# Kernel tuning notes

Hardware: AMD Instinct MI355X
Metric: run time of the kernel (lower is better)

Reference implementation:

```python
import jax, jax.numpy as jnp
import numpy as np

C = 256
NUM_HEADS = 8
EPS = 1e-5


def setup_inputs() -> dict:
    key = jax.random.key(0)
    ks = jax.random.split(key, 8)
    x = jax.random.normal(ks[0], (2, C, 64, 64), dtype=jnp.float32)
    # LayerNorm params (torch default: weight=1, bias=0)
    norm_w = jnp.ones((C,), jnp.float32)
    norm_b = jnp.zeros((C,), jnp.float32)
    # qkv Linear: weight (3C, C), bias (3C,)
    qkv_w = jax.random.normal(ks[1], (3 * C, C), dtype=jnp.float32) * (1.0 / np.sqrt(C))
    qkv_b = jax.random.normal(ks[2], (3 * C,), dtype=jnp.float32) * 0.01
    # proj Linear: weight (C, C), bias (C,)
    proj_w = jax.random.normal(ks[3], (C, C), dtype=jnp.float32) * (1.0 / np.sqrt(C))
    proj_b = jax.random.normal(ks[4], (C,), dtype=jnp.float32) * 0.01
    # gamma initialized to zeros in torch, but use small nonzero so output depends on attention
    gamma = jnp.full((1,), 0.1, jnp.float32)
    return {"x": x, "norm_w": norm_w, "norm_b": norm_b, "qkv_w": qkv_w,
            "qkv_b": qkv_b, "proj_w": proj_w, "proj_b": proj_b, "gamma": gamma}


def reference(x, norm_w, norm_b, qkv_w, qkv_b, proj_w, proj_b, gamma):
    B, Cc, H, W = x.shape
    N = H * W
    nh = NUM_HEADS
    hd = Cc // nh
    scale = hd ** (-0.5)

    # (B, N, C)
    x_flat = x.reshape(B, Cc, N).transpose(0, 2, 1)

    # LayerNorm over last dim
    mu = jnp.mean(x_flat, axis=-1, keepdims=True)
    var = jnp.mean(jnp.square(x_flat - mu), axis=-1, keepdims=True)
    x_norm = (x_flat - mu) * jax.lax.rsqrt(var + EPS) * norm_w + norm_b

    # QKV projection: (B, N, 3C) -> (3, B, nh, N, hd)
    qkv = x_norm @ qkv_w.T + qkv_b
    qkv = qkv.reshape(B, N, 3, nh, hd).transpose(2, 0, 3, 1, 4)
    q, k, v = qkv[0], qkv[1], qkv[2]

    # attention scores (B, nh, N, N); note torch code scales AFTER q@k.T
    attn = jnp.einsum('bhnd,bhmd->bhnm', q, k) * scale
    attn = jax.nn.softmax(attn, axis=-1)

    # (B, nh, N, hd) -> (B, N, C)
    x_attn = jnp.einsum('bhnm,bhmd->bhnd', attn, v)
    x_attn = x_attn.transpose(0, 2, 1, 3).reshape(B, N, Cc)
    x_attn = x_attn @ proj_w.T + proj_b

    # back to (B, C, H, W) and scaled residual
    x_attn = x_attn.transpose(0, 2, 1).reshape(B, Cc, H, W)
    return gamma * x_attn + x
```

## Files before the change

kernel.cpp:

```cpp
#include <hip/hip_runtime.h>

#define CCH   256
#define NSEQ  4096
#define NH    8
#define HD    32

typedef short s8x __attribute__((ext_vector_type(8)));
typedef float f4x __attribute__((ext_vector_type(4)));

__device__ __forceinline__ f4x mfma16(s8x a, s8x b, f4x c) {
  return __builtin_amdgcn_mfma_f32_16x16x32_bf16(a, b, c, 0, 0, 0);
}

__device__ __forceinline__ unsigned short f2bf(float f) {
  union { float f; unsigned int u; } v; v.f = f;
  unsigned int u = v.u + 0x7fffu + ((v.u >> 16) & 1u);
  return (unsigned short)(u >> 16);
}

__device__ __forceinline__ unsigned int pk_bf_rnd(float lo, float hi) {
  return (unsigned int)f2bf(lo) | ((unsigned int)f2bf(hi) << 16);
}

__device__ __forceinline__ unsigned int pk_bf_trunc(float lo, float hi) {
  union { float f; unsigned int u; } a, b; a.f = lo; b.f = hi;
  return __builtin_amdgcn_perm(b.u, a.u, 0x07060302);
}

#if defined(__has_builtin)
#if __has_builtin(__builtin_amdgcn_exp2f)
#define FEXP2(x) __builtin_amdgcn_exp2f(x)
#endif
#endif
#ifndef FEXP2
__device__ __forceinline__ float __fexp2_asm(float x) {
  float r; asm("v_exp_f32 %0, %1" : "=v"(r) : "v"(x)); return r;
}
#define FEXP2(x) __fexp2_asm(x)
#endif

#define C2SCALE (0.17677669529663689f * 1.4426950408889634f)

__global__ __launch_bounds__(256) void ln_cvt_kernel(const float* __restrict__ x,
                                                     const float* __restrict__ nw,
                                                     const float* __restrict__ nb,
                                                     unsigned short* __restrict__ xn,
                                                     const float* __restrict__ qw,
                                                     const float* __restrict__ pw,
                                                     unsigned short* __restrict__ qwb,
                                                     unsigned short* __restrict__ pwb) {
  if (blockIdx.x >= 256) {
    const int t = (blockIdx.x - 256) * 256 + threadIdx.x;
    const float4* src;
    unsigned short* dst;
    int idx;
    if (t < 49152) { src = reinterpret_cast<const float4*>(qw); dst = qwb; idx = t; }
    else           { src = reinterpret_cast<const float4*>(pw); dst = pwb; idx = t - 49152; }
    const float4 vv = src[idx];
    union { unsigned short u[4]; uint2 v; } pk;
    pk.u[0] = f2bf(vv.x); pk.u[1] = f2bf(vv.y); pk.u[2] = f2bf(vv.z); pk.u[3] = f2bf(vv.w);
    *reinterpret_cast<uint2*>(dst + 4 * idx) = pk.v;
    return;
  }

  __shared__ float Ls[256 * 32];
  __shared__ float Sred[2][32][8];
  __shared__ float Mrs[32][2];
  const int t  = threadIdx.x;
  const int n  = t & 31;
  const int cg = t >> 5;
  const int p0 = blockIdx.x * 32;
  const int b  = p0 >> 12;
  const int n0 = p0 & 4095;
  const float* xb = x + (size_t)b * CCH * NSEQ + n0;

  #pragma unroll
  for (int i = 0; i < 32; ++i) {
    const int c = i * 8 + cg;
    Ls[c * 32 + (n ^ (c & 31))] = xb[(size_t)c * NSEQ + n];
  }
  __syncthreads();

  float s = 0.f, sq = 0.f;
  #pragma unroll
  for (int j = 0; j < 32; ++j) {
    const int c = cg * 32 + j;
    const float v = Ls[c * 32 + (n ^ j)];
    s += v; sq += v * v;
  }
  Sred[0][n][cg] = s; Sred[1][n][cg] = sq;
  __syncthreads();
  float ts = 0.f, tq = 0.f;
  #pragma unroll
  for (int g = 0; g < 8; ++g) { ts += Sred[0][n][g]; tq += Sred[1][n][g]; }
  const float mean = ts * (1.f / 256.f);
  const float rstd = rsqrtf(tq * (1.f / 256.f) - mean * mean + 1e-5f);
  if (cg == 0) { Mrs[n][0] = mean; Mrs[n][1] = rstd; }
  __syncthreads();

  const int n2  = t >> 3;
  const int c8b = t & 7;
  const float mean2 = Mrs[n2][0];
  const float rstd2 = Mrs[n2][1];
  unsigned short* orow = xn + ((size_t)b * NSEQ + n0 + n2) * CCH;
  #pragma unroll
  for (int j8 = 0; j8 < 4; ++j8) {
    const int cb = (j8 * 8 + c8b) * 8;
    unsigned int w_[4];
    #pragma unroll
    for (int hw = 0; hw < 4; ++hw) {
      const int c = cb + hw * 2;
      const float v0 = Ls[c * 32 + (n2 ^ (c & 31))];
      const float v1 = Ls[(c + 1) * 32 + (n2 ^ ((c + 1) & 31))];
      const float y0 = (v0 - mean2) * rstd2 * nw[c] + nb[c];
      const float y1 = (v1 - mean2) * rstd2 * nw[c + 1] + nb[c + 1];
      w_[hw] = pk_bf_rnd(y0, y1);
    }
    uint4 pkv; pkv.x = w_[0]; pkv.y = w_[1]; pkv.z = w_[2]; pkv.w = w_[3];
    *reinterpret_cast<uint4*>(orow + cb) = pkv;
  }
}

#define GEMM_CORE(A_PTR, B_PTR, ACC)                                            \
  {                                                                             \
    for (int kb = 0; kb < 4; ++kb) {                                            \
      if (kb) __syncthreads();                                                  \
      _Pragma("unroll")                                                         \
      for (int j = 0; j < 4; ++j) {                                             \
        const int c = j * 256 + tid;                                            \
        const int ar = c >> 3, acr = c & 7;                                     \
        *reinterpret_cast<s8x*>(&As[ar * 64 + ((acr ^ (ar & 7)) << 3)]) =       \
          *reinterpret_cast<const s8x*>(A_PTR + (size_t)(mt * 128 + ar) * CCH + kb * 64 + acr * 8); \
      }                                                                         \
      _Pragma("unroll")                                                         \
      for (int j = 0; j < 2; ++j) {                                             \
        const int c = j * 256 + tid;                                            \
        const int br = c >> 3, bcr = c & 7;                                     \
        *reinterpret_cast<s8x*>(&Bs[br * 64 + ((bcr ^ (br & 7)) << 3)]) =       \
          *reinterpret_cast<const s8x*>(B_PTR + (size_t)(nt * 64 + br) * CCH + kb * 64 + bcr * 8); \
      }                                                                         \
      __syncthreads();                                                          \
      _Pragma("unroll")                                                         \
      for (int kin = 0; kin < 2; ++kin) {                                       \
        const int chx = ((kin * 4 + quad) ^ (l16 & 7)) << 3;                    \
        const s8x a0 = *reinterpret_cast<const s8x*>(&As[(wv * 32 + l16) * 64 + chx]);      \
        const s8x a1 = *reinterpret_cast<const s8x*>(&As[(wv * 32 + 16 + l16) * 64 + chx]); \
        _Pragma("unroll")                                                       \
        for (int ni = 0; ni < 4; ++ni) {                                        \
          const s8x bf = *reinterpret_cast<const s8x*>(&Bs[(ni * 16 + l16) * 64 + chx]);    \
          ACC[0][ni] = mfma16(a0, bf, ACC[0][ni]);                              \
          ACC[1][ni] = mfma16(a1, bf, ACC[1][ni]);                              \
        }                                                                       \
      }                                                                         \
    }                                                                           \
  }

__global__ __launch_bounds__(256, 3) void qkv_gemm(const unsigned short* __restrict__ xn,
                                                   const unsigned short* __restrict__ w,
                                                   const float* __restrict__ bias,
                                                   unsigned short* __restrict__ q,
                                                   unsigned short* __restrict__ k,
                                                   unsigned short* __restrict__ vt) {
  __shared__ unsigned short As[128 * 64];
  __shared__ unsigned short Bs[64 * 64];
  __shared__ unsigned short Ts[128 * 72];
  const int tid = threadIdx.x;
  const int wv  = tid >> 6;
  const int lane = tid & 63;
  const int quad = lane >> 4, l16 = lane & 15;
  const int mt = blockIdx.x;
  const int nt = blockIdx.y;

  f4x acc[2][4];
  #pragma unroll
  for (int mi = 0; mi < 2; ++mi)
    #pragma unroll
    for (int ni = 0; ni < 4; ++ni)
      acc[mi][ni] = (f4x){0.f, 0.f, 0.f, 0.f};

  GEMM_CORE(xn, w, acc)

  const int sel = nt >> 2;
  if (sel == 2) {
    #pragma unroll
    for (int ni = 0; ni < 4; ++ni) {
      const int o = nt * 64 + ni * 16 + l16;
      const float bs = bias[o];
      const int ol = o & 255;
      const int head = ol >> 5, d = ol & 31;
      #pragma unroll
      for (int mi = 0; mi < 2; ++mi) {
        const int g0 = mt * 128 + wv * 32 + mi * 16 + quad * 4;
        const int bb = g0 >> 12, n0 = g0 & 4095;
        unsigned short* vp = vt + ((size_t)(bb * NH + head) * HD + d) * NSEQ + n0;
        uint2 pk;
        pk.x = pk_bf_rnd(acc[mi][ni][0] + bs, acc[mi][ni][1] + bs);
        pk.y = pk_bf_rnd(acc[mi][ni][2] + bs, acc[mi][ni][3] + bs);
        *reinterpret_cast<uint2*>(vp) = pk;
      }
    }
  } else {
    const float sc = (sel == 0) ? C2SCALE : 1.f;
    unsigned short* base = (sel == 0) ? q : k;
    #pragma unroll
    for (int ni = 0; ni < 4; ++ni) {
      const int o = nt * 64 + ni * 16 + l16;
      const float bs = bias[o];
      const int oc = ni * 16 + l16;
      #pragma unroll
      for (int mi = 0; mi < 2; ++mi) {
        const int nl = wv * 32 + mi * 16 + quad * 4;
        #pragma unroll
        for (int r = 0; r < 4; ++r)
          Ts[(nl + r) * 72 + oc] = f2bf((acc[mi][ni][r] + bs) * sc);
      }
    }
    const int n2 = tid >> 1;
    const int hh = tid & 1;
    const int head = 2 * (nt & 3) + hh;
    const int g = mt * 128 + n2;
    const int bb = g >> 12, n0g = g & 4095;
    unsigned short* dst = base + ((size_t)(bb * NH + head) * NSEQ + n0g) * HD;
    #pragma unroll
    for (int j = 0; j < 4; ++j) {
      const uint4 v = *reinterpret_cast<const uint4*>(&Ts[n2 * 72 + hh * 32 + j * 8]);
      *reinterpret_cast<uint4*>(dst + j * 8) = v;
    }
  }
}

__global__ __launch_bounds__(256, 3) void proj_gemm(const unsigned short* __restrict__ xa,
                                                    const unsigned short* __restrict__ w,
                                                    const float* __restrict__ bias,
                                                    const float* __restrict__ gamma,
                                                    const float* __restrict__ x,
                                                    float* __restrict__ out) {
  __shared__ unsigned short As[128 * 64];
  __shared__ unsigned short Bs[64 * 64];
  const int tid = threadIdx.x;
  const int wv  = tid >> 6;
  const int lane = tid & 63;
  const int quad = lane >> 4, l16 = lane & 15;
  const int mt = blockIdx.x;
  const int nt = blockIdx.y;

  f4x acc[2][4];
  #pragma unroll
  for (int mi = 0; mi < 2; ++mi)
    #pragma unroll
    for (int ni = 0; ni < 4; ++ni)
      acc[mi][ni] = (f4x){0.f, 0.f, 0.f, 0.f};

  GEMM_CORE(xa, w, acc)

  const float g0 = gamma[0];
  #pragma unroll
  for (int ni = 0; ni < 4; ++ni) {
    const int c = nt * 64 + ni * 16 + l16;
    const float bs = bias[c];
    #pragma unroll
    for (int mi = 0; mi < 2; ++mi) {
      const int gr = mt * 128 + wv * 32 + mi * 16 + quad * 4;
      const int bb = gr >> 12, n0 = gr & 4095;
      const size_t off = (size_t)(bb * CCH + c) * NSEQ + n0;
      const float4 xv = *reinterpret_cast<const float4*>(x + off);
      float4 ov;
      ov.x = g0 * (acc[mi][ni][0] + bs) + xv.x;
      ov.y = g0 * (acc[mi][ni][1] + bs) + xv.y;
      ov.z = g0 * (acc[mi][ni][2] + bs) + xv.z;
      ov.w = g0 * (acc[mi][ni][3] + bs) + xv.w;
      *reinterpret_cast<float4*>(out + off) = ov;
    }
  }
}

__global__ __launch_bounds__(256, 4) void fa_kernel(const unsigned short* __restrict__ q,
                                                    const unsigned short* __restrict__ k,
                                                    const unsigned short* __restrict__ vt,
                                                    float* __restrict__ Opart,
                                                    float* __restrict__ Lpart) {
  __shared__ unsigned short Ks[2][64 * 40];
  __shared__ unsigned short Vs[2][32 * 72];
  __shared__ unsigned short Ps[128 * 72];

  const int tid  = threadIdx.x;
  const int wv   = tid >> 6;
  const int lane = tid & 63;
  const int quad = lane >> 4;
  const int l16  = lane & 15;
  const int i    = blockIdx.x;
  const int bh   = i & 15;
  const int rest = i >> 4;
  const int half = rest & 1;
  const int qblk = rest >> 1;
  const int kv0  = half * 2048;

  const unsigned short* kb_ = k  + ((size_t)bh * NSEQ + kv0) * HD;
  const unsigned short* vb_ = vt + (size_t)bh * HD * NSEQ + kv0;

  const int krow = tid >> 2;
  const int kdc  = (tid & 3) * 8;
  const int vrow = tid >> 3;
  const int vkc  = (tid & 7) * 8;

  s8x bq0, bq1;
  {
    const unsigned short* qb = q + ((size_t)bh * NSEQ + (size_t)qblk * 128 + wv * 32) * HD;
    bq0 = *reinterpret_cast<const s8x*>(qb + (size_t)l16 * HD + quad * 8);
    bq1 = *reinterpret_cast<const s8x*>(qb + (size_t)(16 + l16) * HD + quad * 8);
  }

  uint4 kreg = *reinterpret_cast<const uint4*>(kb_ + (size_t)krow * HD + kdc);
  uint4 vreg = *reinterpret_cast<const uint4*>(vb_ + (size_t)vrow * NSEQ + vkc);
  *reinterpret_cast<uint4*>(&Ks[0][krow * 40 + kdc]) = kreg;
  *reinterpret_cast<uint4*>(&Vs[0][vrow * 72 + vkc]) = vreg;
  kreg = *reinterpret_cast<const uint4*>(kb_ + (size_t)(64 + krow) * HD + kdc);
  vreg = *reinterpret_cast<const uint4*>(vb_ + (size_t)vrow * NSEQ + 64 + vkc);
  __syncthreads();

  f4x st[4][2];
  #pragma unroll
  for (int ii = 0; ii < 4; ++ii) {
    const s8x ak = *reinterpret_cast<const s8x*>(&Ks[0][(ii * 16 + l16) * 40 + quad * 8]);
    const f4x z = {0.f, 0.f, 0.f, 0.f};
    st[ii][0] = mfma16(ak, bq0, z);
    st[ii][1] = mfma16(ak, bq1, z);
  }

  f4x oacc[2][2];
  #pragma unroll
  for (int dt = 0; dt < 2; ++dt)
    #pragma unroll
    for (int ct = 0; ct < 2; ++ct)
      oacc[dt][ct] = (f4x){0.f, 0.f, 0.f, 0.f};
  f4x accL[2] = {(f4x){0.f, 0.f, 0.f, 0.f}, (f4x){0.f, 0.f, 0.f, 0.f}};

  s8x ones;
  #pragma unroll
  for (int j = 0; j < 8; ++j) ones[j] = (short)0x3F80;

  const int r0 = (wv * 32 + l16) * 72;
  const int r1 = (wv * 32 + 16 + l16) * 72;

  for (int t = 0; t < 32; ++t) {
    const int c = t & 1;

    if (t + 1 < 32) {
      *reinterpret_cast<uint4*>(&Ks[c ^ 1][krow * 40 + kdc]) = kreg;
      *reinterpret_cast<uint4*>(&Vs[c ^ 1][vrow * 72 + vkc]) = vreg;
    }

    #pragma unroll
    for (int ct = 0; ct < 2; ++ct) {
      const int prow = (wv * 32 + ct * 16 + l16) * 72;
      #pragma unroll
      for (int ii = 0; ii < 4; ++ii) {
        const float e0 = FEXP2(st[ii][ct][0]);
        const float e1 = FEXP2(st[ii][ct][1]);
        const float e2 = FEXP2(st[ii][ct][2]);
        const float e3 = FEXP2(st[ii][ct][3]);
        uint2 pw;
        pw.x = pk_bf_trunc(e0, e1);
        pw.y = pk_bf_trunc(e2, e3);
        *reinterpret_cast<uint2*>(&Ps[prow + ii * 16 + quad * 4]) = pw;
      }
    }

    if (t + 2 < 32) {
      kreg = *reinterpret_cast<const uint4*>(kb_ + (size_t)((t + 2) * 64 + krow) * HD + kdc);
      vreg = *reinterpret_cast<const uint4*>(vb_ + (size_t)vrow * NSEQ + (t + 2) * 64 + vkc);
    }

    #pragma unroll
    for (int kb2 = 0; kb2 < 2; ++kb2) {
      const s8x bp0 = *reinterpret_cast<const s8x*>(&Ps[r0 + kb2 * 32 + quad * 8]);
      const s8x bp1 = *reinterpret_cast<const s8x*>(&Ps[r1 + kb2 * 32 + quad * 8]);
      const s8x av0 = *reinterpret_cast<const s8x*>(&Vs[c][l16 * 72 + kb2 * 32 + quad * 8]);
      const s8x av1 = *reinterpret_cast<const s8x*>(&Vs[c][(16 + l16) * 72 + kb2 * 32 + quad * 8]);
      oacc[0][0] = mfma16(av0, bp0, oacc[0][0]);
      oacc[1][0] = mfma16(av1, bp0, oacc[1][0]);
      oacc[0][1] = mfma16(av0, bp1, oacc[0][1]);
      oacc[1][1] = mfma16(av1, bp1, oacc[1][1]);
      accL[0] = mfma16(ones, bp0, accL[0]);
      accL[1] = mfma16(ones, bp1, accL[1]);
    }

    __syncthreads();

    if (t + 1 < 32) {
      #pragma unroll
      for (int ii = 0; ii < 4; ++ii) {
        const s8x ak = *reinterpret_cast<const s8x*>(&Ks[c ^ 1][(ii * 16 + l16) * 40 + quad * 8]);
        const f4x z = {0.f, 0.f, 0.f, 0.f};
        st[ii][0] = mfma16(ak, bq0, z);
        st[ii][1] = mfma16(ak, bq1, z);
      }
    }
  }

  #pragma unroll
  for (int ct = 0; ct < 2; ++ct) {
    const int qg = qblk * 128 + wv * 32 + ct * 16 + l16;
    float* obase = Opart + ((size_t)(half * 16 + bh) * NSEQ + qg) * HD;
    #pragma unroll
    for (int dt = 0; dt < 2; ++dt) {
      float4 ov;
      ov.x = oacc[dt][ct][0]; ov.y = oacc[dt][ct][1];
      ov.z = oacc[dt][ct][2]; ov.w = oacc[dt][ct][3];
      *reinterpret_cast<float4*>(obase + dt * 16 + quad * 4) = ov;
    }
    if (quad == 0)
      Lpart[(size_t)(half * 16 + bh) * NSEQ + qg] = accL[ct][0];
  }
}

__global__ __launch_bounds__(256) void fa_combine(const float* __restrict__ Opart,
                                                  const float* __restrict__ Lpart,
                                                  unsigned short* __restrict__ xa) {
  const int t  = blockIdx.x * 256 + threadIdx.x;
  const int c8 = t & 3;
  const int n  = (t >> 2) & 4095;
  const int bh = t >> 14;
  const int b  = bh >> 3, h = bh & 7;

  const size_t o0 = ((size_t)bh * NSEQ + n) * HD + c8 * 8;
  const size_t o1 = o0 + (size_t)16 * NSEQ * HD;
  const float4 a0 = *reinterpret_cast<const float4*>(Opart + o0);
  const float4 a1 = *reinterpret_cast<const float4*>(Opart + o0 + 4);
  const float4 b0 = *reinterpret_cast<const float4*>(Opart + o1);
  const float4 b1 = *reinterpret_cast<const float4*>(Opart + o1 + 4);
  const float l0 = Lpart[(size_t)bh * NSEQ + n];
  const float l1 = Lpart[(size_t)(16 + bh) * NSEQ + n];
  const float rl = 1.f / (l0 + l1);

  uint4 ow;
  ow.x = pk_bf_rnd((a0.x + b0.x) * rl, (a0.y + b0.y) * rl);
  ow.y = pk_bf_rnd((a0.z + b0.z) * rl, (a0.w + b0.w) * rl);
  ow.z = pk_bf_rnd((a1.x + b1.x) * rl, (a1.y + b1.y) * rl);
  ow.w = pk_bf_rnd((a1.z + b1.z) * rl, (a1.w + b1.w) * rl);
  *reinterpret_cast<uint4*>(xa + ((size_t)b * NSEQ + n) * CCH + h * HD + c8 * 8) = ow;
}

extern "C" void kernel_launch(void* const* d_in, const int* in_sizes, int n_in,
                              void* d_out, int out_size, void* d_ws, size_t ws_size,
                              hipStream_t stream) {
  const float* x      = (const float*)d_in[0];
  const float* norm_w = (const float*)d_in[1];
  const float* norm_b = (const float*)d_in[2];
  const float* qkv_w  = (const float*)d_in[3];
  const float* qkv_b  = (const float*)d_in[4];
  const float* proj_w = (const float*)d_in[5];
  const float* proj_b = (const float*)d_in[6];
  const float* gamma  = (const float*)d_in[7];
  float* out = (float*)d_out;

  char* ws = (char*)d_ws;
  unsigned short* xn  = (unsigned short*)(ws);
  unsigned short* qwb = (unsigned short*)(ws + 4194304);
  unsigned short* pwb = (unsigned short*)(ws + 4587520);
  unsigned short* q   = (unsigned short*)(ws + 4718592);
  unsigned short* k   = (unsigned short*)(ws + 8912896);
  unsigned short* vt  = (unsigned short*)(ws + 13107200);
  unsigned short* xa  = (unsigned short*)(ws + 17301504);
  float* Opart        = (float*)(ws + 21495808);
  float* Lpart        = (float*)(ws + 38273024);

  hipLaunchKernelGGL(ln_cvt_kernel, dim3(512), dim3(256), 0, stream,
                     x, norm_w, norm_b, xn, qkv_w, proj_w, qwb, pwb);
  hipLaunchKernelGGL(qkv_gemm,  dim3(64, 12), dim3(256), 0, stream, xn, qwb, qkv_b, q, k, vt);
  hipLaunchKernelGGL(fa_kernel, dim3(1024), dim3(256), 0, stream, q, k, vt, Opart, Lpart);
  hipLaunchKernelGGL(fa_combine, dim3(1024), dim3(256), 0, stream, Opart, Lpart, xa);
  hipLaunchKernelGGL(proj_gemm, dim3(64, 4), dim3(256), 0, stream, xa, pwb, proj_b, gamma, x, out);
}
```

Before: 155.2 us.

## Double-buffer LDS tiles with register prefetch in QKV and proj GEMMs

Replaces the single-buffered GEMM core with a ping-pong shared-memory scheme where the next K-tile is staged in registers and written to the alternate buffer while the current tile is consumed by MFMAs. Global loads for tile kb+2 are issued during compute of tile kb, which is meant to hide memory latency and remove one barrier per iteration. The QKV kernel reuses the pooled LDS for its transpose staging buffer. The cost is more LDS per block and more registers, which may lower occupancy.

```diff
diff --git a/kernel.cpp b/kernel.cpp
--- a/kernel.cpp
+++ b/kernel.cpp
@@ -121,37 +121,79 @@
   }
 }
 
-#define GEMM_CORE(A_PTR, B_PTR, ACC)                                            \
+#define GEMM_CORE2(A_PTR, B_PTR, ACC)                                           \
   {                                                                             \
+    unsigned short* const As0_ = Pool;                                          \
+    unsigned short* const As1_ = Pool + 8192;                                   \
+    unsigned short* const Bs0_ = Pool + 16384;                                  \
+    unsigned short* const Bs1_ = Pool + 20480;                                  \
+    const int tr = tid >> 3, c8 = tid & 7;                                      \
+    uint4 ra[4], rb[2];                                                         \
+                               \
+    _Pragma("unroll")                                                           \
+    for (int j = 0; j < 4; ++j)                                                 \
+      ra[j] = *reinterpret_cast<const uint4*>(A_PTR + (size_t)(mt * 128 + j * 32 + tr) * CCH + c8 * 8); \
+    _Pragma("unroll")                                                           \
+    for (int j = 0; j < 2; ++j)                                                 \
+      rb[j] = *reinterpret_cast<const uint4*>(B_PTR + (size_t)(nt * 64 + j * 32 + tr) * CCH + c8 * 8);  \
+    _Pragma("unroll")                                                           \
+    for (int j = 0; j < 4; ++j) {                                               \
+      const int ar = j * 32 + tr;                                               \
+      *reinterpret_cast<uint4*>(&As0_[ar * 64 + ((c8 ^ (ar & 7)) << 3)]) = ra[j]; \
+    }                                                                           \
+    _Pragma("unroll")                                                           \
+    for (int j = 0; j < 2; ++j) {                                               \
+      const int br = j * 32 + tr;                                               \
+      *reinterpret_cast<uint4*>(&Bs0_[br * 64 + ((c8 ^ (br & 7)) << 3)]) = rb[j]; \
+    }                                                                           \
+    _Pragma("unroll")                                                           \
+    for (int j = 0; j < 4; ++j)                                                 \
+      ra[j] = *reinterpret_cast<const uint4*>(A_PTR + (size_t)(mt * 128 + j * 32 + tr) * CCH + 64 + c8 * 8); \
+    _Pragma("unroll")                                                           \
+    for (int j = 0; j < 2; ++j)                                                 \
+      rb[j] = *reinterpret_cast<const uint4*>(B_PTR + (size_t)(nt * 64 + j * 32 + tr) * CCH + 64 + c8 * 8);  \
+    __syncthreads();                                                            \
     for (int kb = 0; kb < 4; ++kb) {                                            \
-      if (kb) __syncthreads();                                                  \
-      _Pragma("unroll")                                                         \
-      for (int j = 0; j < 4; ++j) {                                             \
-        const int c = j * 256 + tid;                                            \
-        const int ar = c >> 3, acr = c & 7;                                     \
-        *reinterpret_cast<s8x*>(&As[ar * 64 + ((acr ^ (ar & 7)) << 3)]) =       \
-          *reinterpret_cast<const s8x*>(A_PTR + (size_t)(mt * 128 + ar) * CCH + kb * 64 + acr * 8); \
+      unsigned short* const Asc_ = (kb & 1) ? As1_ : As0_;                      \
+      unsigned short* const Bsc_ = (kb & 1) ? Bs1_ : Bs0_;                      \
+      unsigned short* const Asn_ = (kb & 1) ? As0_ : As1_;                      \
+      unsigned short* const Bsn_ = (kb & 1) ? Bs0_ : Bs1_;                      \
+                                   \
+      if (kb + 1 < 4) {                                                         \
+        _Pragma("unroll")                                                       \
+        for (int j = 0; j < 4; ++j) {                                           \
+          const int ar = j * 32 + tr;                                           \
+          *reinterpret_cast<uint4*>(&Asn_[ar * 64 + ((c8 ^ (ar & 7)) << 3)]) = ra[j]; \
+        }                                                                       \
+        _Pragma("unroll")                                                       \
+        for (int j = 0; j < 2; ++j) {                                           \
+          const int br = j * 32 + tr;                                           \
+          *reinterpret_cast<uint4*>(&Bsn_[br * 64 + ((c8 ^ (br & 7)) << 3)]) = rb[j]; \
+        }                                                                       \
       }                                                                         \
-      _Pragma("unroll")                                                         \
-      for (int j = 0; j < 2; ++j) {                                             \
-        const int c = j * 256 + tid;                                            \
-        const int br = c >> 3, bcr = c & 7;                                     \
-        *reinterpret_cast<s8x*>(&Bs[br * 64 + ((bcr ^ (br & 7)) << 3)]) =       \
-          *reinterpret_cast<const s8x*>(B_PTR + (size_t)(nt * 64 + br) * CCH + kb * 64 + bcr * 8); \
+                       \
+      if (kb + 2 < 4) {                                                         \
+        _Pragma("unroll")                                                       \
+        for (int j = 0; j < 4; ++j)                                             \
+          ra[j] = *reinterpret_cast<const uint4*>(A_PTR + (size_t)(mt * 128 + j * 32 + tr) * CCH + (kb + 2) * 64 + c8 * 8); \
+        _Pragma("unroll")                                                       \
+        for (int j = 0; j < 2; ++j)                                             \
+          rb[j] = *reinterpret_cast<const uint4*>(B_PTR + (size_t)(nt * 64 + j * 32 + tr) * CCH + (kb + 2) * 64 + c8 * 8);  \
       }                                                                         \
-      __syncthreads();                                                          \
+                                                      \
       _Pragma("unroll")                                                         \
       for (int kin = 0; kin < 2; ++kin) {                                       \
         const int chx = ((kin * 4 + quad) ^ (l16 & 7)) << 3;                    \
-        const s8x a0 = *reinterpret_cast<const s8x*>(&As[(wv * 32 + l16) * 64 + chx]);      \
-        const s8x a1 = *reinterpret_cast<const s8x*>(&As[(wv * 32 + 16 + l16) * 64 + chx]); \
+        const s8x a0 = *reinterpret_cast<const s8x*>(&Asc_[(wv * 32 + l16) * 64 + chx]);      \
+        const s8x a1 = *reinterpret_cast<const s8x*>(&Asc_[(wv * 32 + 16 + l16) * 64 + chx]); \
         _Pragma("unroll")                                                       \
         for (int ni = 0; ni < 4; ++ni) {                                        \
-          const s8x bf = *reinterpret_cast<const s8x*>(&Bs[(ni * 16 + l16) * 64 + chx]);    \
+          const s8x bf = *reinterpret_cast<const s8x*>(&Bsc_[(ni * 16 + l16) * 64 + chx]);    \
           ACC[0][ni] = mfma16(a0, bf, ACC[0][ni]);                              \
           ACC[1][ni] = mfma16(a1, bf, ACC[1][ni]);                              \
         }                                                                       \
       }                                                                         \
+      __syncthreads();                                                          \
     }                                                                           \
   }
 
@@ -161,9 +203,7 @@
                                                    unsigned short* __restrict__ q,
                                                    unsigned short* __restrict__ k,
                                                    unsigned short* __restrict__ vt) {
-  __shared__ unsigned short As[128 * 64];
-  __shared__ unsigned short Bs[64 * 64];
-  __shared__ unsigned short Ts[128 * 72];
+  __shared__ __align__(16) unsigned short Pool[24576];
   const int tid = threadIdx.x;
   const int wv  = tid >> 6;
   const int lane = tid & 63;
@@ -178,7 +218,7 @@
     for (int ni = 0; ni < 4; ++ni)
       acc[mi][ni] = (f4x){0.f, 0.f, 0.f, 0.f};
 
-  GEMM_CORE(xn, w, acc)
+  GEMM_CORE2(xn, w, acc)
 
   const int sel = nt >> 2;
   if (sel == 2) {
@@ -200,6 +240,7 @@
       }
     }
   } else {
+    unsigned short* const Ts = Pool;
     const float sc = (sel == 0) ? C2SCALE : 1.f;
     unsigned short* base = (sel == 0) ? q : k;
     #pragma unroll
@@ -235,8 +276,7 @@
                                                     const float* __restrict__ gamma,
                                                     const float* __restrict__ x,
                                                     float* __restrict__ out) {
-  __shared__ unsigned short As[128 * 64];
-  __shared__ unsigned short Bs[64 * 64];
+  __shared__ __align__(16) unsigned short Pool[24576];
   const int tid = threadIdx.x;
   const int wv  = tid >> 6;
   const int lane = tid & 63;
@@ -251,7 +291,7 @@
     for (int ni = 0; ni < 4; ++ni)
       acc[mi][ni] = (f4x){0.f, 0.f, 0.f, 0.f};
 
-  GEMM_CORE(xa, w, acc)
+  GEMM_CORE2(xa, w, acc)
 
   const float g0 = gamma[0];
   #pragma unroll
```

Measured after the change: 173.2 us. 11.6% more time.

## Software-pipeline PV MFMAs one iteration behind exp/P-write in attention loop

Applied to the files above, without the earlier changes.

Moves the P·V and row-sum MFMAs of iteration t into iteration t+1, with the V fragments kept in registers across the barrier. The exp and bf16 packing of the next P tile can then overlap the previous tile's matrix work, and a tail block handles the last tile. The Ps tile is read back at the start of the next iteration, which relies on the barrier for ordering. This costs extra VGPRs for the held V fragments and may change occupancy.

```diff
diff --git a/kernel.cpp b/kernel.cpp
--- a/kernel.cpp
+++ b/kernel.cpp
@@ -342,12 +342,34 @@
   const int r0 = (wv * 32 + l16) * 72;
   const int r1 = (wv * 32 + 16 + l16) * 72;
 
+  s8x vavr[4];
+
   for (int t = 0; t < 32; ++t) {
     const int c = t & 1;
+
+    s8x bp[4];
+    if (t > 0) {
+      bp[0] = *reinterpret_cast<const s8x*>(&Ps[r0 + 0 * 32 + quad * 8]);
+      bp[1] = *reinterpret_cast<const s8x*>(&Ps[r1 + 0 * 32 + quad * 8]);
+      bp[2] = *reinterpret_cast<const s8x*>(&Ps[r0 + 1 * 32 + quad * 8]);
+      bp[3] = *reinterpret_cast<const s8x*>(&Ps[r1 + 1 * 32 + quad * 8]);
+    }
 
     if (t + 1 < 32) {
       *reinterpret_cast<uint4*>(&Ks[c ^ 1][krow * 40 + kdc]) = kreg;
       *reinterpret_cast<uint4*>(&Vs[c ^ 1][vrow * 72 + vkc]) = vreg;
+    }
+
+    if (t > 0) {
+      #pragma unroll
+      for (int kb2 = 0; kb2 < 2; ++kb2) {
+        oacc[0][0] = mfma16(vavr[kb2],     bp[2 * kb2],     oacc[0][0]);
+        oacc[1][0] = mfma16(vavr[2 + kb2], bp[2 * kb2],     oacc[1][0]);
+        oacc[0][1] = mfma16(vavr[kb2],     bp[2 * kb2 + 1], oacc[0][1]);
+        oacc[1][1] = mfma16(vavr[2 + kb2], bp[2 * kb2 + 1], oacc[1][1]);
+        accL[0] = mfma16(ones, bp[2 * kb2],     accL[0]);
+        accL[1] = mfma16(ones, bp[2 * kb2 + 1], accL[1]);
+      }
     }
 
     #pragma unroll
@@ -373,16 +395,8 @@
 
     #pragma unroll
     for (int kb2 = 0; kb2 < 2; ++kb2) {
-      const s8x bp0 = *reinterpret_cast<const s8x*>(&Ps[r0 + kb2 * 32 + quad * 8]);
-      const s8x bp1 = *reinterpret_cast<const s8x*>(&Ps[r1 + kb2 * 32 + quad * 8]);
-      const s8x av0 = *reinterpret_cast<const s8x*>(&Vs[c][l16 * 72 + kb2 * 32 + quad * 8]);
-      const s8x av1 = *reinterpret_cast<const s8x*>(&Vs[c][(16 + l16) * 72 + kb2 * 32 + quad * 8]);
-      oacc[0][0] = mfma16(av0, bp0, oacc[0][0]);
-      oacc[1][0] = mfma16(av1, bp0, oacc[1][0]);
-      oacc[0][1] = mfma16(av0, bp1, oacc[0][1]);
-      oacc[1][1] = mfma16(av1, bp1, oacc[1][1]);
-      accL[0] = mfma16(ones, bp0, accL[0]);
-      accL[1] = mfma16(ones, bp1, accL[1]);
+      vavr[kb2]     = *reinterpret_cast<const s8x*>(&Vs[c][l16 * 72 + kb2 * 32 + quad * 8]);
+      vavr[2 + kb2] = *reinterpret_cast<const s8x*>(&Vs[c][(16 + l16) * 72 + kb2 * 32 + quad * 8]);
     }
 
     __syncthreads();
@@ -395,6 +409,23 @@
         st[ii][0] = mfma16(ak, bq0, z);
         st[ii][1] = mfma16(ak, bq1, z);
       }
+    }
+  }
+
+  {
+    s8x bp[4];
+    bp[0] = *reinterpret_cast<const s8x*>(&Ps[r0 + 0 * 32 + quad * 8]);
+    bp[1] = *reinterpret_cast<const s8x*>(&Ps[r1 + 0 * 32 + quad * 8]);
+    bp[2] = *reinterpret_cast<const s8x*>(&Ps[r0 + 1 * 32 + quad * 8]);
+    bp[3] = *reinterpret_cast<const s8x*>(&Ps[r1 + 1 * 32 + quad * 8]);
+    #pragma unroll
+    for (int kb2 = 0; kb2 < 2; ++kb2) {
+      oacc[0][0] = mfma16(vavr[kb2],     bp[2 * kb2],     oacc[0][0]);
+      oacc[1][0] = mfma16(vavr[2 + kb2], bp[2 * kb2],     oacc[1][0]);
+      oacc[0][1] = mfma16(vavr[kb2],     bp[2 * kb2 + 1], oacc[0][1]);
+      oacc[1][1] = mfma16(vavr[2 + kb2], bp[2 * kb2 + 1], oacc[1][1]);
+      accL[0] = mfma16(ones, bp[2 * kb2],     accL[0]);
+      accL[1] = mfma16(ones, bp[2 * kb2 + 1], accL[1]);
     }
   }
 
```

Measured after the change: 149.4 us. 1.04x faster.
